# Optimization experiments

Hardware: AMD Instinct MI355X
Metric: run time of the kernel (lower is better)

## Reference

```python
import jax, jax.numpy as jnp
import numpy as np

N_NODES = 50000
N_EDGES = 800000
IN_DIM = 256
EMB_DIM = 256
N_COMS = 4
D_COM = EMB_DIM // N_COMS  # 64
BN_EPS = 1e-5


def setup_inputs() -> dict:
    key = jax.random.key(0)
    ks = jax.random.split(key, 16)
    s1 = 1.0 / np.sqrt(IN_DIM)
    s2 = 1.0 / np.sqrt(D_COM)
    return {
        "x": jax.random.normal(ks[0], (N_NODES, IN_DIM), jnp.float32),
        "edge_index": jax.random.randint(ks[1], (2, N_EDGES), 0, N_NODES, jnp.int32),
        "ew": jax.random.uniform(ks[2], (N_COMS, N_EDGES), jnp.float32),
        "W1_0": jax.random.normal(ks[3], (N_COMS, IN_DIM, D_COM), jnp.float32) * s1,
        "b1_0": jnp.zeros((N_COMS, D_COM), jnp.float32),
        "W2_0": jax.random.normal(ks[4], (N_COMS, D_COM, D_COM), jnp.float32) * s2,
        "b2_0": jnp.zeros((N_COMS, D_COM), jnp.float32),
        "g0": jnp.ones((N_COMS, D_COM), jnp.float32),
        "bt0": jnp.zeros((N_COMS, D_COM), jnp.float32),
        "W1_1": jax.random.normal(ks[5], (N_COMS, D_COM, D_COM), jnp.float32) * s2,
        "b1_1": jnp.zeros((N_COMS, D_COM), jnp.float32),
        "W2_1": jax.random.normal(ks[6], (N_COMS, D_COM, D_COM), jnp.float32) * s2,
        "b2_1": jnp.zeros((N_COMS, D_COM), jnp.float32),
        "g1": jnp.ones((N_COMS, D_COM), jnp.float32),
        "bt1": jnp.zeros((N_COMS, D_COM), jnp.float32),
        "encW": jax.random.normal(ks[7], (IN_DIM, EMB_DIM), jnp.float32) * s1,
        "encb": jnp.zeros((EMB_DIM,), jnp.float32),
    }


def _gin_bn_relu(h, src, dst, w, W1, b1, W2, b2, gamma, beta):
    # weighted scatter-add aggregation: agg[i] = sum_{e:(j->i)} w_e * h[j]
    msg = h[src] * w[:, None]                       # [E, F]
    agg = jax.ops.segment_sum(msg, dst, num_segments=N_NODES)
    z = h + agg                                      # eps = 0 (train_eps=False)
    z = jax.nn.relu(z @ W1 + b1) @ W2 + b2           # GIN MLP
    mu = jnp.mean(z, axis=0)
    var = jnp.var(z, axis=0)
    z = gamma * (z - mu) * jax.lax.rsqrt(var + BN_EPS) + beta
    return jax.nn.relu(z)                            # dropout: eval mode no-op


def reference(x, edge_index, ew, W1_0, b1_0, W2_0, b2_0, g0, bt0,
              W1_1, b1_1, W2_1, b2_1, g1, bt1, encW, encb):
    src, dst = edge_index[0], edge_index[1]
    outs1, outs2 = [], []
    for k in range(N_COMS):
        h1 = _gin_bn_relu(x, src, dst, ew[k], W1_0[k], b1_0[k], W2_0[k], b2_0[k], g0[k], bt0[k])
        h2 = _gin_bn_relu(h1, src, dst, ew[k], W1_1[k], b1_1[k], W2_1[k], b2_1[k], g1[k], bt1[k])
        outs1.append(h1)
        outs2.append(h2)
    out1 = jnp.concatenate(outs1, axis=-1)  # [N, emb_dim]
    out2 = jnp.concatenate(outs2, axis=-1)  # [N, emb_dim]
    enc = x @ encW + encb                   # input_encoder
    return (enc, out1, out2)
```

## Files before the change

kernel.cpp:

```cpp
#include <hip/hip_runtime.h>

#define NN 50000
#define NE 800000
#define FDIM 256
#define SCAN_BLOCKS 196
#define MMG 782
#define G32 1563

typedef __attribute__((ext_vector_type(8))) short short8v;
typedef __attribute__((ext_vector_type(4))) float float4v;

__device__ __forceinline__ unsigned short f2bf(float f) {
  unsigned u = __float_as_uint(f);
  unsigned r = (u + 0x7fffu + ((u >> 16) & 1u)) >> 16;
  return (unsigned short)r;
}
__device__ __forceinline__ float bf2f(unsigned short b) {
  return __uint_as_float(((unsigned)b) << 16);
}


__global__ __launch_bounds__(256) void k_hist(const int* __restrict__ dst, int* __restrict__ deg16,
                                              int* __restrict__ rank) {
  int e = blockIdx.x * 256 + threadIdx.x;
  if (e < NE) rank[e] = atomicAdd(&deg16[dst[e] << 4], 1);
}

__device__ __forceinline__ int block_incl_scan(int v, int* wsum) {
  const int tid = threadIdx.x;
  const int lane = tid & 63;
  const int w = tid >> 6;
  int incl = v;
  #pragma unroll
  for (int off = 1; off < 64; off <<= 1) {
    int tmp = __shfl_up(incl, off, 64);
    if (lane >= off) incl += tmp;
  }
  if (lane == 63) wsum[w] = incl;
  __syncthreads();
  int woff = 0;
  #pragma unroll
  for (int k = 0; k < 3; k++)
    if (k < w) woff += wsum[k];
  return woff + incl;
}

__global__ __launch_bounds__(256) void k_scan_a(const int* __restrict__ deg16, int* __restrict__ partial) {
  __shared__ int wsum[4];
  int i = blockIdx.x * 256 + threadIdx.x;
  int v = (i < NN) ? deg16[i << 4] : 0;
  int incl = block_incl_scan(v, wsum);
  if (threadIdx.x == 255) partial[blockIdx.x] = incl;
}

__global__ __launch_bounds__(256) void k_scanb_wprep(int* __restrict__ partial, int* __restrict__ offs,
                                                     const float* __restrict__ W1_0, const float* __restrict__ encW,
                                                     const float* __restrict__ W1_1, const float* __restrict__ W2_0,
                                                     const float* __restrict__ W2_1, unsigned short* __restrict__ Bt1,
                                                     unsigned short* __restrict__ BtE, unsigned short* __restrict__ Wb11,
                                                     unsigned short* __restrict__ Wb20, unsigned short* __restrict__ Wb21) {
  if (blockIdx.x == 256) {
    __shared__ int wsum[4];
    int tid = threadIdx.x;
    int v = (tid < SCAN_BLOCKS) ? partial[tid] : 0;
    int incl = block_incl_scan(v, wsum);
    if (tid < SCAN_BLOCKS) partial[tid] = incl - v;
    if (tid == 255) offs[NN] = incl;
    return;
  }
  const int t = blockIdx.x;
  const int k = threadIdx.x;
  const int c = t >> 6, j = t & 63;
  Bt1[t * 256 + k] = f2bf(W1_0[c * 16384 + k * 64 + j]);
  BtE[t * 256 + k] = f2bf(encW[k * 256 + t]);
  if (k < 64) {
    Wb11[c * 4096 + j * 64 + k] = f2bf(W1_1[c * 4096 + k * 64 + j]);
    Wb20[c * 4096 + j * 64 + k] = f2bf(W2_0[c * 4096 + k * 64 + j]);
    Wb21[c * 4096 + j * 64 + k] = f2bf(W2_1[c * 4096 + k * 64 + j]);
  }
}

__global__ __launch_bounds__(256) void k_scan_c(const int* __restrict__ deg16, const int* __restrict__ partial,
                                                int* __restrict__ offs) {
  __shared__ int wsum[4];
  int i = blockIdx.x * 256 + threadIdx.x;
  int v = (i < NN) ? deg16[i << 4] : 0;
  int incl = block_incl_scan(v, wsum);
  int excl = partial[blockIdx.x] + incl - v;
  if (i < NN) offs[i] = excl;
}

__global__ __launch_bounds__(256) void k_fill(const int* __restrict__ srcA, const int* __restrict__ dstA,
                                              const float* __restrict__ ew, const int* __restrict__ rank,
                                              const int* __restrict__ offs, int4* __restrict__ recs) {
  int e = blockIdx.x * 256 + threadIdx.x;
  if (e < NE) {
    int sA = srcA[e];
    int dA = dstA[e];
    int rk = rank[e];
    unsigned p01 = (unsigned)f2bf(ew[e]) | ((unsigned)f2bf(ew[NE + e]) << 16);
    unsigned p23 = (unsigned)f2bf(ew[2 * NE + e]) | ((unsigned)f2bf(ew[3 * NE + e]) << 16);
    recs[offs[dA] + rk] = make_int4(sA, (int)p01, (int)p23, 0);
  }
}

__global__ __launch_bounds__(256) void k_mm(const float* __restrict__ x,
                                            const unsigned short* __restrict__ Bt1,
                                            const unsigned short* __restrict__ BtE,
                                            const float* __restrict__ encb,
                                            unsigned short* __restrict__ Pout,
                                            float* __restrict__ encout) {
  __shared__ __align__(16) unsigned short xs[32][264];
  const int tid = threadIdx.x;
  const int lane = tid & 63;
  const int w = tid >> 6;
  const int isE = blockIdx.y;
  const int colw = w * 64;
  const int row0 = blockIdx.x * 32;
  const int lr = lane & 15;
  const int lk = (lane >> 4) * 8;
  const int rbase = (lane >> 4) * 4;

  const unsigned short* Bt = isE ? BtE : Bt1;
  const unsigned short* Bptr[4];
  #pragma unroll
  for (int ct = 0; ct < 4; ct++) Bptr[ct] = Bt + (size_t)(colw + ct * 16 + lr) * 256 + lk;

  short8v bcur[4];
  #pragma unroll
  for (int ct = 0; ct < 4; ct++) bcur[ct] = *reinterpret_cast<const short8v*>(Bptr[ct]);

  float4 xv[8];
  #pragma unroll
  for (int it = 0; it < 8; it++) {
    int idx = it * 256 + tid;
    int grow = row0 + (idx >> 6);
    if (grow >= NN) grow = NN - 1;
    xv[it] = *reinterpret_cast<const float4*>(x + (size_t)grow * 256 + (idx & 63) * 4);
  }
  #pragma unroll
  for (int it = 0; it < 8; it++) {
    int idx = it * 256 + tid;
    ushort4 o;
    o.x = f2bf(xv[it].x); o.y = f2bf(xv[it].y); o.z = f2bf(xv[it].z); o.w = f2bf(xv[it].w);
    *reinterpret_cast<ushort4*>(&xs[idx >> 6][(idx & 63) * 4]) = o;
  }
  __syncthreads();

  float4v acc[2][4];
  #pragma unroll
  for (int rt = 0; rt < 2; rt++)
    #pragma unroll
    for (int ct = 0; ct < 4; ct++) acc[rt][ct] = (float4v){0.f, 0.f, 0.f, 0.f};

  #pragma unroll
  for (int ks8 = 0; ks8 < 8; ks8++) {
    const int ks = ks8 * 32;
    short8v bnxt[4];
    if (ks8 < 7) {
      #pragma unroll
      for (int ct = 0; ct < 4; ct++) bnxt[ct] = *reinterpret_cast<const short8v*>(Bptr[ct] + ks + 32);
    }
    short8v a[2];
    #pragma unroll
    for (int rt = 0; rt < 2; rt++)
      a[rt] = *reinterpret_cast<const short8v*>(&xs[rt * 16 + lr][ks + lk]);
    #pragma unroll
    for (int rt = 0; rt < 2; rt++)
      #pragma unroll
      for (int ct = 0; ct < 4; ct++)
        acc[rt][ct] = __builtin_amdgcn_mfma_f32_16x16x32_bf16(a[rt], bcur[ct], acc[rt][ct], 0, 0, 0);
    if (ks8 < 7) {
      #pragma unroll
      for (int ct = 0; ct < 4; ct++) bcur[ct] = bnxt[ct];
    }
  }

  __syncthreads();
  if (!isE) {
    #pragma unroll
    for (int rt = 0; rt < 2; rt++)
      #pragma unroll
      for (int ct = 0; ct < 4; ct++) {
        const int col = colw + ct * 16 + lr;
        #pragma unroll
        for (int r = 0; r < 4; r++) xs[rt * 16 + rbase + r][col] = f2bf(acc[rt][ct][r]);
      }
    __syncthreads();
    #pragma unroll
    for (int it = 0; it < 4; it++) {
      int idx = it * 256 + tid;
      int row = idx >> 5;
      int p = idx & 31;
      if (row0 + row < NN)
        *reinterpret_cast<short8v*>(Pout + (size_t)(row0 + row) * 256 + p * 8) =
            *reinterpret_cast<const short8v*>(&xs[row][p * 8]);
    }
  } else {
    float bv[4];
    #pragma unroll
    for (int ct = 0; ct < 4; ct++) bv[ct] = encb[colw + ct * 16 + lr];
    float (*cs)[132] = reinterpret_cast<float(*)[132]>(&xs[0][0]);
    #pragma unroll
    for (int ph = 0; ph < 2; ph++) {
      if ((colw >> 7) == ph) {
        #pragma unroll
        for (int rt = 0; rt < 2; rt++)
          #pragma unroll
          for (int ct = 0; ct < 4; ct++) {
            const int col = colw + ct * 16 + lr - ph * 128;
            #pragma unroll
            for (int r = 0; r < 4; r++) cs[rt * 16 + rbase + r][col] = acc[rt][ct][r] + bv[ct];
          }
      }
      __syncthreads();
      #pragma unroll
      for (int it = 0; it < 4; it++) {
        int idx = it * 256 + tid;
        int row = idx >> 5;
        int p = idx & 31;
        if (row0 + row < NN)
          *reinterpret_cast<float4*>(encout + (size_t)(row0 + row) * 256 + ph * 128 + p * 4) =
              *reinterpret_cast<const float4*>(&cs[row][p * 4]);
      }
      __syncthreads();
    }
  }
}

__global__ __launch_bounds__(256) void k_agg(const unsigned short* __restrict__ P,
                                             const int* __restrict__ offs, const int4* __restrict__ recs,
                                             const float* __restrict__ b1, unsigned short* __restrict__ Rb) {
  const int lane = threadIdx.x & 63;
  const int wid = threadIdx.x >> 6;
  const int i = blockIdx.x * 4 + wid;
  const int half = lane >> 5;
  const int l32 = lane & 31;
  const int col0 = l32 * 8;
  const int c = l32 >> 3;

  const int es = offs[i], ee = offs[i + 1];
  float acc[8];
  #pragma unroll
  for (int j = 0; j < 8; j++) acc[j] = 0.f;

  for (int base = es; base < ee; base += 16) {
    int sq[8];
    float wq[8];
    #pragma unroll
    for (int q = 0; q < 8; q++) {
      int e = base + 2 * q + half;
      bool valid = e < ee;
      int4 rv = recs[valid ? e : es];
      sq[q] = rv.x;
      unsigned p = (c < 2) ? (unsigned)rv.y : (unsigned)rv.z;
      unsigned short wb = (c & 1) ? (unsigned short)(p >> 16) : (unsigned short)(p & 0xffff);
      wq[q] = valid ? bf2f(wb) : 0.f;
    }
    short8v pq[8];
    #pragma unroll
    for (int q = 0; q < 8; q++)
      pq[q] = *reinterpret_cast<const short8v*>(P + (size_t)sq[q] * 256 + col0);
    #pragma unroll
    for (int q = 0; q < 8; q++)
      #pragma unroll
      for (int j = 0; j < 8; j++)
        acc[j] = fmaf(wq[q], bf2f((unsigned short)pq[q][j]), acc[j]);
  }

  #pragma unroll
  for (int j = 0; j < 8; j++) acc[j] += __shfl_xor(acc[j], 32);

  if (half == 0) {
    short8v ps = *reinterpret_cast<const short8v*>(P + (size_t)i * 256 + col0);
    float4 b4a = *reinterpret_cast<const float4*>(b1 + col0);
    float4 b4b = *reinterpret_cast<const float4*>(b1 + col0 + 4);
    float bb[8] = {b4a.x, b4a.y, b4a.z, b4a.w, b4b.x, b4b.y, b4b.z, b4b.w};
    short8v out;
    #pragma unroll
    for (int j = 0; j < 8; j++) {
      float r = bf2f((unsigned short)ps[j]) + acc[j] + bb[j];
      out[j] = (short)f2bf(r > 0.f ? r : 0.f);
    }
    *reinterpret_cast<short8v*>(Rb + (size_t)i * 256 + col0) = out;
  }
}

__global__ __launch_bounds__(256) void k_bd_stats(const unsigned short* __restrict__ A,
                                                  const unsigned short* __restrict__ Wz,
                                                  float* __restrict__ bnsum, float* __restrict__ bnsq) {
  const int lane = threadIdx.x & 63;
  const int c = threadIdx.x >> 6;
  const int row0 = blockIdx.x * 64;
  const int lr = lane & 15;
  const int lk = (lane >> 4) * 8;

  const unsigned short* Aptr[4];
  #pragma unroll
  for (int rt = 0; rt < 4; rt++) {
    int row = row0 + rt * 16 + lr;
    if (row >= NN) row = NN - 1;
    Aptr[rt] = A + (size_t)row * 256 + c * 64 + lk;
  }

  float4v acc[4][4];
  #pragma unroll
  for (int rt = 0; rt < 4; rt++)
    #pragma unroll
    for (int ct = 0; ct < 4; ct++) acc[rt][ct] = (float4v){0.f, 0.f, 0.f, 0.f};

  #pragma unroll
  for (int ks = 0; ks < 64; ks += 32) {
    short8v a[4], b[4];
    #pragma unroll
    for (int rt = 0; rt < 4; rt++) a[rt] = *reinterpret_cast<const short8v*>(Aptr[rt] + ks);
    #pragma unroll
    for (int ct = 0; ct < 4; ct++)
      b[ct] = *reinterpret_cast<const short8v*>(Wz + (size_t)c * 4096 + (ct * 16 + lr) * 64 + ks + lk);
    #pragma unroll
    for (int rt = 0; rt < 4; rt++)
      #pragma unroll
      for (int ct = 0; ct < 4; ct++)
        acc[rt][ct] = __builtin_amdgcn_mfma_f32_16x16x32_bf16(a[rt], b[ct], acc[rt][ct], 0, 0, 0);
  }

  #pragma unroll
  for (int ct = 0; ct < 4; ct++) {
    const int col = c * 64 + ct * 16 + lr;
    float s1 = 0.f, s2 = 0.f;
    #pragma unroll
    for (int rt = 0; rt < 4; rt++) {
      #pragma unroll
      for (int r = 0; r < 4; r++) {
        const int row = row0 + rt * 16 + (lane >> 4) * 4 + r;
        if (row < NN) {
          float v = acc[rt][ct][r];
          s1 += v;
          s2 += v * v;
        }
      }
    }
    s1 += __shfl_xor(s1, 16); s1 += __shfl_xor(s1, 32);
    s2 += __shfl_xor(s2, 16); s2 += __shfl_xor(s2, 32);
    if (lane < 16) {
      atomicAdd(&bnsum[col], s1);
      atomicAdd(&bnsq[col], s2);
    }
  }
}

template <int WITH_P2>
__global__ __launch_bounds__(256) void k_bd_bn(const unsigned short* __restrict__ A,
                                               const unsigned short* __restrict__ Wz,
                                               const float* __restrict__ bnsum, const float* __restrict__ bnsq,
                                               const float* __restrict__ g, const float* __restrict__ bt,
                                               const unsigned short* __restrict__ Wp,
                                               float* __restrict__ Hout, unsigned short* __restrict__ P2out) {
  __shared__ __align__(16) unsigned short h_lds[64][264];
  const int lane = threadIdx.x & 63;
  const int c = threadIdx.x >> 6;
  const int row0 = blockIdx.x * 64;
  const int lr = lane & 15;
  const int lk = (lane >> 4) * 8;
  const int rbase = (lane >> 4) * 4;

  const unsigned short* Aptr[4];
  #pragma unroll
  for (int rt = 0; rt < 4; rt++) {
    int row = row0 + rt * 16 + lr;
    if (row >= NN) row = NN - 1;
    Aptr[rt] = A + (size_t)row * 256 + c * 64 + lk;
  }

  float4v acc[4][4];
  #pragma unroll
  for (int rt = 0; rt < 4; rt++)
    #pragma unroll
    for (int ct = 0; ct < 4; ct++) acc[rt][ct] = (float4v){0.f, 0.f, 0.f, 0.f};

  #pragma unroll
  for (int ks = 0; ks < 64; ks += 32) {
    short8v a[4], b[4];
    #pragma unroll
    for (int rt = 0; rt < 4; rt++) a[rt] = *reinterpret_cast<const short8v*>(Aptr[rt] + ks);
    #pragma unroll
    for (int ct = 0; ct < 4; ct++)
      b[ct] = *reinterpret_cast<const short8v*>(Wz + (size_t)c * 4096 + (ct * 16 + lr) * 64 + ks + lk);
    #pragma unroll
    for (int rt = 0; rt < 4; rt++)
      #pragma unroll
      for (int ct = 0; ct < 4; ct++)
        acc[rt][ct] = __builtin_amdgcn_mfma_f32_16x16x32_bf16(a[rt], b[ct], acc[rt][ct], 0, 0, 0);
  }

  float sc[4], sh[4];
  #pragma unroll
  for (int ct = 0; ct < 4; ct++) {
    const int t = c * 64 + ct * 16 + lr;
    float mu = bnsum[t] * (1.f / NN);
    float var = bnsq[t] * (1.f / NN) - mu * mu;
    var = var > 0.f ? var : 0.f;
    float rs = rsqrtf(var + 1e-5f);
    sc[ct] = g[t] * rs;
    sh[ct] = bt[t] - mu * sc[ct];
  }

  #pragma unroll
  for (int rt = 0; rt < 4; rt++) {
    #pragma unroll
    for (int ct = 0; ct < 4; ct++) {
      const int col = c * 64 + ct * 16 + lr;
      #pragma unroll
      for (int r = 0; r < 4; r++) {
        const int rowl = rt * 16 + rbase + r;
        const int row = row0 + rowl;
        float h = fmaf(acc[rt][ct][r], sc[ct], sh[ct]);
        h = h > 0.f ? h : 0.f;
        if (row < NN) Hout[(size_t)row * 256 + col] = h;
        if (WITH_P2) h_lds[rowl][col] = f2bf(h);
      }
    }
  }

  if (WITH_P2) {
    __syncthreads();
    float4v acc2[4][4];
    #pragma unroll
    for (int rt = 0; rt < 4; rt++)
      #pragma unroll
      for (int ct = 0; ct < 4; ct++) acc2[rt][ct] = (float4v){0.f, 0.f, 0.f, 0.f};
    #pragma unroll
    for (int ks = 0; ks < 64; ks += 32) {
      short8v a[4], b[4];
      #pragma unroll
      for (int rt = 0; rt < 4; rt++)
        a[rt] = *reinterpret_cast<const short8v*>(&h_lds[rt * 16 + lr][c * 64 + ks + lk]);
      #pragma unroll
      for (int ct = 0; ct < 4; ct++)
        b[ct] = *reinterpret_cast<const short8v*>(Wp + (size_t)c * 4096 + (ct * 16 + lr) * 64 + ks + lk);
      #pragma unroll
      for (int rt = 0; rt < 4; rt++)
        #pragma unroll
        for (int ct = 0; ct < 4; ct++)
          acc2[rt][ct] = __builtin_amdgcn_mfma_f32_16x16x32_bf16(a[rt], b[ct], acc2[rt][ct], 0, 0, 0);
    }
    #pragma unroll
    for (int rt = 0; rt < 4; rt++) {
      #pragma unroll
      for (int ct = 0; ct < 4; ct++) {
        const int col = c * 64 + ct * 16 + lr;
        #pragma unroll
        for (int r = 0; r < 4; r++) {
          const int row = row0 + rt * 16 + rbase + r;
          if (row < NN) P2out[(size_t)row * 256 + col] = f2bf(acc2[rt][ct][r]);
        }
      }
    }
  }
}


extern "C" void kernel_launch(void* const* d_in, const int* in_sizes, int n_in,
                              void* d_out, int out_size, void* d_ws, size_t ws_size,
                              hipStream_t stream) {
  const float* x    = (const float*)d_in[0];
  const int*   ei   = (const int*)d_in[1];
  const float* ew   = (const float*)d_in[2];
  const float* W1_0 = (const float*)d_in[3];
  const float* b1_0 = (const float*)d_in[4];
  const float* W2_0 = (const float*)d_in[5];
  const float* g0   = (const float*)d_in[7];
  const float* bt0  = (const float*)d_in[8];
  const float* W1_1 = (const float*)d_in[9];
  const float* b1_1 = (const float*)d_in[10];
  const float* W2_1 = (const float*)d_in[11];
  const float* g1   = (const float*)d_in[13];
  const float* bt1  = (const float*)d_in[14];
  const float* encW = (const float*)d_in[15];
  const float* encb = (const float*)d_in[16];

  const int* srcA = ei;
  const int* dstA = ei + NE;

  float* out_enc = (float*)d_out;
  float* out1 = out_enc + (size_t)NN * FDIM;
  float* out2 = out1 + (size_t)NN * FDIM;

  unsigned short* P1bf = (unsigned short*)out1;
  unsigned short* P2bf = (unsigned short*)out2;

  char* wp = (char*)d_ws;
  auto carve = [&](size_t bytes) {
    char* r = wp;
    wp += (bytes + 255) & ~(size_t)255;
    return r;
  };
  int*   deg16   = (int*)carve((size_t)NN * 16 * 4);
  float* bnsum0  = (float*)carve(256 * 4);
  float* bnsq0   = (float*)carve(256 * 4);
  float* bnsum1  = (float*)carve(256 * 4);
  float* bnsq1   = (float*)carve(256 * 4);
  int*   offs    = (int*)carve((size_t)(NN + 1) * 4);
  int*   rank    = (int*)carve((size_t)NE * 4);
  int*   partial = (int*)carve(SCAN_BLOCKS * 4);
  unsigned short* Bt1  = (unsigned short*)carve(256 * 256 * 2);
  unsigned short* BtE  = (unsigned short*)carve(256 * 256 * 2);
  unsigned short* Wb11 = (unsigned short*)carve(4 * 64 * 64 * 2);
  unsigned short* Wb20 = (unsigned short*)carve(4 * 64 * 64 * 2);
  unsigned short* Wb21 = (unsigned short*)carve(4 * 64 * 64 * 2);
  int4* recs           = (int4*)carve((size_t)NE * 16);
  unsigned short* Rb   = (unsigned short*)carve((size_t)NN * FDIM * 2);

  const size_t zspan = (((size_t)NN * 16 * 4 + 255) & ~(size_t)255) + 4 * 1024;
  hipMemsetAsync(deg16, 0, zspan, stream);

  k_hist<<<(NE + 255) / 256, 256, 0, stream>>>(dstA, deg16, rank);
  k_scan_a<<<SCAN_BLOCKS, 256, 0, stream>>>(deg16, partial);
  k_scanb_wprep<<<257, 256, 0, stream>>>(partial, offs, W1_0, encW, W1_1, W2_0, W2_1,
                                         Bt1, BtE, Wb11, Wb20, Wb21);
  k_scan_c<<<SCAN_BLOCKS, 256, 0, stream>>>(deg16, partial, offs);

  k_fill<<<(NE + 255) / 256, 256, 0, stream>>>(srcA, dstA, ew, rank, offs, recs);

  k_mm<<<dim3(G32, 2), 256, 0, stream>>>(x, Bt1, BtE, encb, P1bf, out_enc);

  k_agg<<<NN / 4, 256, 0, stream>>>(P1bf, offs, recs, b1_0, Rb);
  k_bd_stats<<<MMG, 256, 0, stream>>>(Rb, Wb20, bnsum0, bnsq0);
  k_bd_bn<1><<<MMG, 256, 0, stream>>>(Rb, Wb20, bnsum0, bnsq0, g0, bt0, Wb11, out1, P2bf);

  k_agg<<<NN / 4, 256, 0, stream>>>(P2bf, offs, recs, b1_1, Rb);
  k_bd_stats<<<MMG, 256, 0, stream>>>(Rb, Wb21, bnsum1, bnsq1);
  k_bd_bn<0><<<MMG, 256, 0, stream>>>(Rb, Wb21, bnsum1, bnsq1, g1, bt1, nullptr, out2, nullptr);
}
```

Baseline: 350.7 us.

## Make input GEMM persistent with register-resident B and double-buffered x tiles

The x@W GEMM kernel becomes persistent over a grid of 256x2 blocks. Each block loads its full B fragment set into registers once and loops over row tiles, prefetching the next x tile into a second LDS buffer while the current one computes. The histogram kernel also processes four edges per thread with fewer blocks. The aim is to cut repeated B loads and launch/tail overhead and to hide global load latency, at the cost of much higher register pressure (32 short8 B fragments plus the prefetch registers) and possibly lower occupancy.

After: 337.8 us. -3.7%, faster.

```diff
diff --git a/kernel.cpp b/kernel.cpp
--- a/kernel.cpp
+++ b/kernel.cpp
@@ -5,7 +5,9 @@
 #define FDIM 256
 #define SCAN_BLOCKS 196
 #define MMG 782
-#define G32 1563
+#define NTILE 1563
+#define GRIDX 256
+#define HIST_BLOCKS 782
 
 typedef __attribute__((ext_vector_type(8))) short short8v;
 typedef __attribute__((ext_vector_type(4))) float float4v;
@@ -22,8 +24,12 @@
 
 __global__ __launch_bounds__(256) void k_hist(const int* __restrict__ dst, int* __restrict__ deg16,
                                               int* __restrict__ rank) {
-  int e = blockIdx.x * 256 + threadIdx.x;
-  if (e < NE) rank[e] = atomicAdd(&deg16[dst[e] << 4], 1);
+  const int base = blockIdx.x * 1024 + threadIdx.x;
+  #pragma unroll
+  for (int k = 0; k < 4; k++) {
+    int e = base + k * 256;
+    if (e < NE) rank[e] = atomicAdd(&deg16[dst[e] << 4], 1);
+  }
 }
 
 __device__ __forceinline__ int block_incl_scan(int v, int* wsum) {
@@ -110,109 +116,102 @@
                                             const float* __restrict__ encb,
                                             unsigned short* __restrict__ Pout,
                                             float* __restrict__ encout) {
-  __shared__ __align__(16) unsigned short xs[32][264];
+  __shared__ __align__(16) unsigned short xs[2][32][264];
   const int tid = threadIdx.x;
   const int lane = tid & 63;
   const int w = tid >> 6;
   const int isE = blockIdx.y;
   const int colw = w * 64;
-  const int row0 = blockIdx.x * 32;
   const int lr = lane & 15;
   const int lk = (lane >> 4) * 8;
   const int rbase = (lane >> 4) * 4;
 
   const unsigned short* Bt = isE ? BtE : Bt1;
-  const unsigned short* Bptr[4];
-  #pragma unroll
-  for (int ct = 0; ct < 4; ct++) Bptr[ct] = Bt + (size_t)(colw + ct * 16 + lr) * 256 + lk;
-
-  short8v bcur[4];
-  #pragma unroll
-  for (int ct = 0; ct < 4; ct++) bcur[ct] = *reinterpret_cast<const short8v*>(Bptr[ct]);
-
-  float4 xv[8];
-  #pragma unroll
-  for (int it = 0; it < 8; it++) {
-    int idx = it * 256 + tid;
-    int grow = row0 + (idx >> 6);
-    if (grow >= NN) grow = NN - 1;
-    xv[it] = *reinterpret_cast<const float4*>(x + (size_t)grow * 256 + (idx & 63) * 4);
-  }
-  #pragma unroll
-  for (int it = 0; it < 8; it++) {
-    int idx = it * 256 + tid;
-    ushort4 o;
-    o.x = f2bf(xv[it].x); o.y = f2bf(xv[it].y); o.z = f2bf(xv[it].z); o.w = f2bf(xv[it].w);
-    *reinterpret_cast<ushort4*>(&xs[idx >> 6][(idx & 63) * 4]) = o;
+
+  short8v bfrag[8][4];
+  #pragma unroll
+  for (int ks8 = 0; ks8 < 8; ks8++)
+    #pragma unroll
+    for (int ct = 0; ct < 4; ct++)
+      bfrag[ks8][ct] = *reinterpret_cast<const short8v*>(
+          Bt + (size_t)(colw + ct * 16 + lr) * 256 + ks8 * 32 + lk);
+
+  float bv[4];
+  #pragma unroll
+  for (int ct = 0; ct < 4; ct++) bv[ct] = isE ? encb[colw + ct * 16 + lr] : 0.f;
+
+  {
+    const int row0 = blockIdx.x * 32;
+    #pragma unroll
+    for (int it = 0; it < 8; it++) {
+      int idx = it * 256 + tid;
+      int grow = row0 + (idx >> 6);
+      if (grow >= NN) grow = NN - 1;
+      float4 v = *reinterpret_cast<const float4*>(x + (size_t)grow * 256 + (idx & 63) * 4);
+      ushort4 o;
+      o.x = f2bf(v.x); o.y = f2bf(v.y); o.z = f2bf(v.z); o.w = f2bf(v.w);
+      *reinterpret_cast<ushort4*>(&xs[0][idx >> 6][(idx & 63) * 4]) = o;
+    }
   }
   __syncthreads();
 
-  float4v acc[2][4];
-  #pragma unroll
-  for (int rt = 0; rt < 2; rt++)
-    #pragma unroll
-    for (int ct = 0; ct < 4; ct++) acc[rt][ct] = (float4v){0.f, 0.f, 0.f, 0.f};
-
-  #pragma unroll
-  for (int ks8 = 0; ks8 < 8; ks8++) {
-    const int ks = ks8 * 32;
-    short8v bnxt[4];
-    if (ks8 < 7) {
-      #pragma unroll
-      for (int ct = 0; ct < 4; ct++) bnxt[ct] = *reinterpret_cast<const short8v*>(Bptr[ct] + ks + 32);
-    }
-    short8v a[2];
+  int cur = 0;
+  for (int t = blockIdx.x; t < NTILE; t += GRIDX, cur ^= 1) {
+    const int row0 = t * 32;
+    const int t2 = t + GRIDX;
+    const bool hasNext = t2 < NTILE;
+
+    float4 xv[8];
+    if (hasNext) {
+      #pragma unroll
+      for (int it = 0; it < 8; it++) {
+        int idx = it * 256 + tid;
+        int grow = t2 * 32 + (idx >> 6);
+        if (grow >= NN) grow = NN - 1;
+        xv[it] = *reinterpret_cast<const float4*>(x + (size_t)grow * 256 + (idx & 63) * 4);
+      }
+    }
+
+    float4v acc[2][4];
     #pragma unroll
     for (int rt = 0; rt < 2; rt++)
-      a[rt] = *reinterpret_cast<const short8v*>(&xs[rt * 16 + lr][ks + lk]);
-    #pragma unroll
-    for (int rt = 0; rt < 2; rt++)
-      #pragma unroll
-      for (int ct = 0; ct < 4; ct++)
-        acc[rt][ct] = __builtin_amdgcn_mfma_f32_16x16x32_bf16(a[rt], bcur[ct], acc[rt][ct], 0, 0, 0);
-    if (ks8 < 7) {
-      #pragma unroll
-      for (int ct = 0; ct < 4; ct++) bcur[ct] = bnxt[ct];
-    }
-  }
-
-  __syncthreads();
-  if (!isE) {
-    #pragma unroll
-    for (int rt = 0; rt < 2; rt++)
-      #pragma unroll
-      for (int ct = 0; ct < 4; ct++) {
-        const int col = colw + ct * 16 + lr;
+      #pragma unroll
+      for (int ct = 0; ct < 4; ct++) acc[rt][ct] = (float4v){0.f, 0.f, 0.f, 0.f};
+
+    #pragma unroll
+    for (int ks8 = 0; ks8 < 8; ks8++) {
+      short8v a[2];
+      #pragma unroll
+      for (int rt = 0; rt < 2; rt++)
+        a[rt] = *reinterpret_cast<const short8v*>(&xs[cur][rt * 16 + lr][ks8 * 32 + lk]);
+      #pragma unroll
+      for (int rt = 0; rt < 2; rt++)
         #pragma unroll
-        for (int r = 0; r < 4; r++) xs[rt * 16 + rbase + r][col] = f2bf(acc[rt][ct][r]);
-      }
+        for (int ct = 0; ct < 4; ct++)
+          acc[rt][ct] = __builtin_amdgcn_mfma_f32_16x16x32_bf16(a[rt], bfrag[ks8][ct], acc[rt][ct], 0, 0, 0);
+    }
+
     __syncthreads();
-    #pragma unroll
-    for (int it = 0; it < 4; it++) {
-      int idx = it * 256 + tid;
-      int row = idx >> 5;
-      int p = idx & 31;
-      if (row0 + row < NN)
-        *reinterpret_cast<short8v*>(Pout + (size_t)(row0 + row) * 256 + p * 8) =
-            *reinterpret_cast<const short8v*>(&xs[row][p * 8]);
-    }
-  } else {
-    float bv[4];
-    #pragma unroll
-    for (int ct = 0; ct < 4; ct++) bv[ct] = encb[colw + ct * 16 + lr];
-    float (*cs)[132] = reinterpret_cast<float(*)[132]>(&xs[0][0]);
-    #pragma unroll
-    for (int ph = 0; ph < 2; ph++) {
-      if ((colw >> 7) == ph) {
+
+    if (hasNext) {
+      #pragma unroll
+      for (int it = 0; it < 8; it++) {
+        int idx = it * 256 + tid;
+        ushort4 o;
+        o.x = f2bf(xv[it].x); o.y = f2bf(xv[it].y); o.z = f2bf(xv[it].z); o.w = f2bf(xv[it].w);
+        *reinterpret_cast<ushort4*>(&xs[cur ^ 1][idx >> 6][(idx & 63) * 4]) = o;
+      }
+    }
+
+    if (!isE) {
+      #pragma unroll
+      for (int rt = 0; rt < 2; rt++)
         #pragma unroll
-        for (int rt = 0; rt < 2; rt++)
+        for (int ct = 0; ct < 4; ct++) {
+          const int col = colw + ct * 16 + lr;
           #pragma unroll
-          for (int ct = 0; ct < 4; ct++) {
-            const int col = colw + ct * 16 + lr - ph * 128;
-            #pragma unroll
-            for (int r = 0; r < 4; r++) cs[rt * 16 + rbase + r][col] = acc[rt][ct][r] + bv[ct];
-          }
-      }
+          for (int r = 0; r < 4; r++) xs[cur][rt * 16 + rbase + r][col] = f2bf(acc[rt][ct][r]);
+        }
       __syncthreads();
       #pragma unroll
       for (int it = 0; it < 4; it++) {
@@ -220,10 +219,35 @@
         int row = idx >> 5;
         int p = idx & 31;
         if (row0 + row < NN)
-          *reinterpret_cast<float4*>(encout + (size_t)(row0 + row) * 256 + ph * 128 + p * 4) =
-              *reinterpret_cast<const float4*>(&cs[row][p * 4]);
-      }
-      __syncthreads();
+          *reinterpret_cast<short8v*>(Pout + (size_t)(row0 + row) * 256 + p * 8) =
+              *reinterpret_cast<const short8v*>(&xs[cur][row][p * 8]);
+      }
+    } else {
+      float (*cs)[132] = reinterpret_cast<float(*)[132]>(&xs[cur][0][0]);
+      #pragma unroll
+      for (int ph = 0; ph < 2; ph++) {
+        if ((colw >> 7) == ph) {
+          #pragma unroll
+          for (int rt = 0; rt < 2; rt++)
+            #pragma unroll
+            for (int ct = 0; ct < 4; ct++) {
+              const int col = colw + ct * 16 + lr - ph * 128;
+              #pragma unroll
+              for (int r = 0; r < 4; r++) cs[rt * 16 + rbase + r][col] = acc[rt][ct][r] + bv[ct];
+            }
+        }
+        __syncthreads();
+        #pragma unroll
+        for (int it = 0; it < 4; it++) {
+          int idx = it * 256 + tid;
+          int row = idx >> 5;
+          int p = idx & 31;
+          if (row0 + row < NN)
+            *reinterpret_cast<float4*>(encout + (size_t)(row0 + row) * 256 + ph * 128 + p * 4) =
+                *reinterpret_cast<const float4*>(&cs[row][p * 4]);
+        }
+        __syncthreads();
+      }
     }
   }
 }
@@ -514,7 +538,7 @@
   const size_t zspan = (((size_t)NN * 16 * 4 + 255) & ~(size_t)255) + 4 * 1024;
   hipMemsetAsync(deg16, 0, zspan, stream);
 
-  k_hist<<<(NE + 255) / 256, 256, 0, stream>>>(dstA, deg16, rank);
+  k_hist<<<HIST_BLOCKS, 256, 0, stream>>>(dstA, deg16, rank);
   k_scan_a<<<SCAN_BLOCKS, 256, 0, stream>>>(deg16, partial);
   k_scanb_wprep<<<257, 256, 0, stream>>>(partial, offs, W1_0, encW, W1_1, W2_0, W2_1,
                                          Bt1, BtE, Wb11, Wb20, Wb21);
@@ -522,7 +546,7 @@
 
   k_fill<<<(NE + 255) / 256, 256, 0, stream>>>(srcA, dstA, ew, rank, offs, recs);
 
-  k_mm<<<dim3(G32, 2), 256, 0, stream>>>(x, Bt1, BtE, encb, P1bf, out_enc);
+  k_mm<<<dim3(GRIDX, 2), 256, 0, stream>>>(x, Bt1, BtE, encb, P1bf, out_enc);
 
   k_agg<<<NN / 4, 256, 0, stream>>>(P1bf, offs, recs, b1_0, Rb);
   k_bd_stats<<<MMG, 256, 0, stream>>>(Rb, Wb20, bnsum0, bnsq0);
```
